# Performance work log

Hardware: AMD Instinct MI355X
Metric: run time of the kernel (lower is better)

The kernel has to match this reference:

```python
import jax, jax.numpy as jnp
import numpy as np

NUM_USERS = 100000
NUM_ITEMS = 50000
N_NODES = NUM_USERS + NUM_ITEMS
DIM = 64
N_LAYERS = 3
NNZ = 1000000
BATCH = 4096


def setup_inputs() -> dict:
    key = jax.random.key(0)
    k = jax.random.split(key, 7)
    user_idx = jax.random.randint(k[0], (BATCH,), 0, NUM_USERS, dtype=jnp.int64 if jax.config.jax_enable_x64 else jnp.int32)
    item_idx = jax.random.randint(k[1], (BATCH,), 0, NUM_ITEMS, dtype=jnp.int64 if jax.config.jax_enable_x64 else jnp.int32)
    rows = jax.random.randint(k[2], (NNZ,), 0, N_NODES, dtype=jnp.int32)
    cols = jax.random.randint(k[3], (NNZ,), 0, N_NODES, dtype=jnp.int32)
    values = jax.random.uniform(k[4], (NNZ,), dtype=jnp.float32)
    # embeddings initialized N(0, 1/dim) as in the torch module
    user_emb = jax.random.normal(k[5], (NUM_USERS, DIM), dtype=jnp.float32) / DIM
    item_emb = jax.random.normal(k[6], (NUM_ITEMS, DIM), dtype=jnp.float32) / DIM
    return {"user_idx": user_idx, "item_idx": item_idx, "rows": rows,
            "cols": cols, "values": values, "user_emb": user_emb, "item_emb": item_emb}


def _spmm(rows, cols, values, x):
    # sparse [N,N] @ dense [N,d] via gather + segment_sum
    gathered = values[:, None] * x[cols]            # [nnz, d]
    return jax.ops.segment_sum(gathered, rows, num_segments=N_NODES)


def _propagate(rows, cols, values, user_emb, item_emb):
    all_emb = jnp.concatenate([user_emb, item_emb], axis=0)  # [N, d]
    acc = all_emb
    for _ in range(N_LAYERS):
        all_emb = _spmm(rows, cols, values, all_emb)
        acc = acc + all_emb
    light_out = acc / jnp.asarray(N_LAYERS + 1, dtype=acc.dtype)  # mean over layers
    return light_out[:NUM_USERS], light_out[NUM_USERS:]


def reference(user_idx, item_idx, rows, cols, values, user_emb, item_emb):
    all_users, all_items = _propagate(rows, cols, values, user_emb, item_emb)
    user = all_users[user_idx]                      # [B, d]
    item = all_items[item_idx]                      # [B, d]
    rating = jnp.sum(user * item, axis=1)           # [B]
    return (rating, user, item)
```

## Files before the change

kernel.cpp:

```cpp
#include <hip/hip_runtime.h>

#define NUM_USERS 100000
#define NUM_ITEMS 50000
#define N_NODES   150000
#define DIM       64
#define NNZ       1000000
#define BATCH     4096

#define BROWS  240
#define NBUCK  (N_NODES / BROWS)
#define WPB    (BROWS / 8)
#define NWG    256
#define CHUNK  ((NNZ + NWG - 1) / NWG)
#define SCAN_N (NBUCK * NWG)
#define SCAN_B 512
#define NBLK_S ((SCAN_N + SCAN_B - 1) / SCAN_B)

#define NWAVES (NBUCK * WPB)
#define NBINS  32
#define ESCAP  4096
#define PACKED_CAP 3000000
#define CVB    2048

typedef unsigned int uint32;

__device__ __forceinline__ ushort f2bf(float f) {
    uint32 u = __float_as_uint(f);
    u += 0x7FFFu + ((u >> 16) & 1u);
    return (ushort)(u >> 16);
}
__device__ __forceinline__ float bf2f(ushort u) {
    return __uint_as_float(((uint32)u) << 16);
}

__global__ __launch_bounds__(256) void count_convert_kernel(
        const int* __restrict__ rows,
        int* __restrict__ cntArr,
        const float* __restrict__ user_emb,
        const float* __restrict__ item_emb,
        ushort* __restrict__ xb) {
    __shared__ int h[NBUCK];
    if (blockIdx.x < NWG) {
        for (int k = threadIdx.x; k < NBUCK; k += 256) h[k] = 0;
        __syncthreads();
        int lo = blockIdx.x * CHUNK, hi = min(NNZ, lo + CHUNK);
        for (int e = lo + threadIdx.x; e < hi; e += 256)
            atomicAdd(&h[__builtin_nontemporal_load(&rows[e]) / BROWS], 1);
        __syncthreads();
        for (int k = threadIdx.x; k < NBUCK; k += 256)
            cntArr[k * NWG + blockIdx.x] = h[k];
    } else {
        const int64_t total4 = (int64_t)N_NODES * DIM / 4;
        const int64_t user4  = (int64_t)NUM_USERS * DIM / 4;
        int64_t stride = (int64_t)CVB * 256;
        for (int64_t i = (int64_t)(blockIdx.x - NWG) * 256 + threadIdx.x;
             i < total4; i += stride) {
            float4 v = (i < user4) ? ((const float4*)user_emb)[i]
                                   : ((const float4*)item_emb)[i - user4];
            ushort4 o;
            o.x = f2bf(v.x); o.y = f2bf(v.y); o.z = f2bf(v.z); o.w = f2bf(v.w);
            ((ushort4*)xb)[i] = o;
        }
    }
}

__global__ __launch_bounds__(SCAN_B) void scan_block_kernel(
        const int* __restrict__ in, int* __restrict__ out,
        int* __restrict__ blksum, int n) {
    __shared__ int sh[SCAN_B];
    int i = blockIdx.x * SCAN_B + threadIdx.x;
    int v = (i < n) ? in[i] : 0;
    sh[threadIdx.x] = v;
    __syncthreads();
    for (int off = 1; off < SCAN_B; off <<= 1) {
        int t = (threadIdx.x >= off) ? sh[threadIdx.x - off] : 0;
        __syncthreads();
        sh[threadIdx.x] += t;
        __syncthreads();
    }
    if (i < n) out[i] = sh[threadIdx.x] - v;
    if (threadIdx.x == SCAN_B - 1) blksum[blockIdx.x] = sh[SCAN_B - 1];
}

__global__ __launch_bounds__(SCAN_B) void scan_top_kernel(int* __restrict__ blksum,
                                                          int nblk,
                                                          int* __restrict__ rowptr,
                                                          int* __restrict__ gcur) {
    __shared__ int sh[SCAN_B];
    int v = (threadIdx.x < nblk) ? blksum[threadIdx.x] : 0;
    sh[threadIdx.x] = v;
    __syncthreads();
    for (int off = 1; off < SCAN_B; off <<= 1) {
        int t = (threadIdx.x >= off) ? sh[threadIdx.x - off] : 0;
        __syncthreads();
        sh[threadIdx.x] += t;
        __syncthreads();
    }
    if (threadIdx.x < nblk) blksum[threadIdx.x] = sh[threadIdx.x] - v;
    if (threadIdx.x == 0) { rowptr[N_NODES] = NNZ; gcur[0] = 0; }
}

__global__ __launch_bounds__(256) void scatter_lds_kernel(
        const int* __restrict__ rows,
        const int* __restrict__ cols,
        const float* __restrict__ vals,
        const int* __restrict__ baseArr,
        const int* __restrict__ blksum,
        int2* __restrict__ ebuf) {
    __shared__ int cur[NBUCK];
    for (int k = threadIdx.x; k < NBUCK; k += 256) {
        int idx = k * NWG + blockIdx.x;
        cur[k] = baseArr[idx] + blksum[idx >> 9];
    }
    __syncthreads();
    int lo = blockIdx.x * CHUNK, hi = min(NNZ, lo + CHUNK);
    for (int e = lo + threadIdx.x; e < hi; e += 256) {
        int   r = __builtin_nontemporal_load(&rows[e]);
        int   c = __builtin_nontemporal_load(&cols[e]);
        float v = __builtin_nontemporal_load(&vals[e]);
        int   b = r / BROWS;
        int pos = atomicAdd(&cur[b], 1);
        ebuf[pos] = make_int2(((r - b * BROWS) << 18) | c, __float_as_int(v));
    }
}

__global__ __launch_bounds__(256) void buildpack_kernel(
        const int* __restrict__ baseArr,
        const int* __restrict__ blksum,
        const int2* __restrict__ ebuf,
        int2* __restrict__ ebuf2,
        int* __restrict__ rowptr,
        int* __restrict__ perm,
        int* __restrict__ tw,
        int* __restrict__ twb,
        int2* __restrict__ packed,
        int* __restrict__ gcur) {
    __shared__ int  cnt[BROWS];
    __shared__ int  rowofs[BROWS];
    __shared__ int  cur[BROWS];
    __shared__ int  sh[256];
    __shared__ int2 es[ESCAP];
    __shared__ int  sr[BROWS];
    __shared__ int  binc[NBINS];
    __shared__ int  binb[NBINS];
    __shared__ int  twq[WPB];
    __shared__ int  lofs[WPB];
    __shared__ int  baseSh;

    const int b   = blockIdx.x;
    const int tid = threadIdx.x;
    const int i0  = b * NWG;
    const int start = baseArr[i0] + blksum[i0 >> 9];
    const int i1  = (b + 1) * NWG;
    const int end = (b == NBUCK - 1) ? NNZ : (baseArr[i1] + blksum[i1 >> 9]);
    const int m   = end - start;

    for (int k = tid; k < BROWS; k += 256) cnt[k] = 0;
    if (tid < NBINS) binc[tid] = 0;
    __syncthreads();

    for (int e = start + tid; e < end; e += 256)
        atomicAdd(&cnt[ebuf[e].x >> 18], 1);
    __syncthreads();

    int v = (tid < BROWS) ? cnt[tid] : 0;
    sh[tid] = v;
    __syncthreads();
    for (int off = 1; off < 256; off <<= 1) {
        int t = (tid >= off) ? sh[tid - off] : 0;
        __syncthreads();
        sh[tid] += t;
        __syncthreads();
    }
    if (tid < BROWS) {
        int p = sh[tid] - v;
        rowofs[tid] = p;
        cur[tid] = p;
        rowptr[b * BROWS + tid] = start + p;
    }
    __syncthreads();

    for (int e = start + tid; e < end; e += 256) {
        int2 p = ebuf[e];
        int row8 = p.x >> 18;
        int col  = p.x & 0x3FFFF;
        int pos = atomicAdd(&cur[row8], 1);
        if (pos < ESCAP) es[pos] = make_int2(col, p.y);
    }
    __syncthreads();
    for (int k = tid; k < m; k += 256) ebuf2[start + k] = es[k];

    if (tid < BROWS) atomicAdd(&binc[min(cnt[tid], NBINS - 1)], 1);
    __syncthreads();
    if (tid == 0) {
        int s = 0;
        for (int k = 0; k < NBINS; ++k) { binb[k] = s; s += binc[k]; binc[k] = 0; }
    }
    __syncthreads();
    if (tid < BROWS) {
        int bin = min(cnt[tid], NBINS - 1);
        int idx = atomicAdd(&binc[bin], 1);
        sr[binb[bin] + idx] = tid;
    }
    __syncthreads();

    if (tid < WPB) {
        int T = 0;
        #pragma unroll
        for (int j = 0; j < 8; ++j) T = max(T, cnt[sr[8 * tid + j]]);
        twq[tid] = T;
    }
    __syncthreads();
    if (tid == 0) {
        int s = 0;
        for (int q = 0; q < WPB; ++q) { lofs[q] = s; s += twq[q]; }
        baseSh = atomicAdd(gcur, s);
    }
    __syncthreads();
    const int base = baseSh;

    if (tid < WPB) {
        tw[b * WPB + tid]  = twq[tid];
        twb[b * WPB + tid] = base + lofs[tid];
    }
    if (tid < BROWS) perm[b * BROWS + tid] = b * BROWS + sr[tid];

    for (int q = 0; q < WPB; ++q) {
        int T = twq[q];
        int64_t bq = (int64_t)(base + lofs[q]) * 8;
        for (int idx = tid; idx < 8 * T; idx += 256) {
            int t = idx >> 3, j = idx & 7;
            int row8 = sr[8 * q + j];
            int d = cnt[row8];
            int2 ed = (t < d) ? es[rowofs[row8] + t] : make_int2(0, 0);
            packed[bq + idx] = ed;
        }
    }
}

__global__ __launch_bounds__(256) void spmm8p_kernel(
        const int* __restrict__ perm,
        const int* __restrict__ twb,
        const int* __restrict__ tw,
        const long long* __restrict__ packed,
        const ushort* __restrict__ xin,
        ushort* __restrict__ yout) {
    int w = (int)((blockIdx.x * blockDim.x + threadIdx.x) >> 6);
    if (w >= NWAVES) return;
    const int lane = threadIdx.x & 63;
    const int j    = lane >> 3;
    const int sub8 = lane & 7;
    const int T = tw[w];
    const int64_t base = (int64_t)twb[w] * 8;
    const int rowv = perm[8 * w + j];
    const uint4* __restrict__ x4 = (const uint4*)xin;

    float acc[8] = {0.f, 0.f, 0.f, 0.f, 0.f, 0.f, 0.f, 0.f};

    #define DO_TRIP(tt)                                                        \
    {                                                                          \
        int   colsel = __shfl(edc, (tt) * 8 + j, 64);                          \
        float valsel = __uint_as_float((uint32)__shfl(edv, (tt) * 8 + j, 64)); \
        uint4 u = x4[(uint32)colsel * 8 + sub8];                               \
        acc[0] = fmaf(valsel, __uint_as_float(u.x << 16), acc[0]);             \
        acc[1] = fmaf(valsel, __uint_as_float(u.x & 0xFFFF0000u), acc[1]);     \
        acc[2] = fmaf(valsel, __uint_as_float(u.y << 16), acc[2]);             \
        acc[3] = fmaf(valsel, __uint_as_float(u.y & 0xFFFF0000u), acc[3]);     \
        acc[4] = fmaf(valsel, __uint_as_float(u.z << 16), acc[4]);             \
        acc[5] = fmaf(valsel, __uint_as_float(u.z & 0xFFFF0000u), acc[5]);     \
        acc[6] = fmaf(valsel, __uint_as_float(u.w << 16), acc[6]);             \
        acc[7] = fmaf(valsel, __uint_as_float(u.w & 0xFFFF0000u), acc[7]);     \
    }

    int t0 = 0;
    for (; t0 + 8 <= T; t0 += 8) {
        long long raw = __builtin_nontemporal_load(&packed[base + (int64_t)t0 * 8 + lane]);
        int edc = (int)(uint32)(raw & 0xFFFFFFFFll);
        int edv = (int)(uint32)(raw >> 32);
        DO_TRIP(0) DO_TRIP(1) DO_TRIP(2) DO_TRIP(3)
        DO_TRIP(4) DO_TRIP(5) DO_TRIP(6) DO_TRIP(7)
    }
    if (t0 < T) {
        long long raw = __builtin_nontemporal_load(&packed[base + (int64_t)t0 * 8 + lane]);
        int edc = (int)(uint32)(raw & 0xFFFFFFFFll);
        int edv = (int)(uint32)(raw >> 32);
        int rem = T - t0;
        for (int tt = 0; tt < rem; ++tt) DO_TRIP(tt)
    }
    #undef DO_TRIP

    uint4 o;
    o.x = (uint32)f2bf(acc[0]) | ((uint32)f2bf(acc[1]) << 16);
    o.y = (uint32)f2bf(acc[2]) | ((uint32)f2bf(acc[3]) << 16);
    o.z = (uint32)f2bf(acc[4]) | ((uint32)f2bf(acc[5]) << 16);
    o.w = (uint32)f2bf(acc[6]) | ((uint32)f2bf(acc[7]) << 16);
    ((uint4*)yout)[(uint32)rowv * 8 + sub8] = o;
}

__global__ __launch_bounds__(256) void batch_out_kernel(
        const int* __restrict__ user_idx,
        const int* __restrict__ item_idx,
        const int* __restrict__ rowptr,
        const int2* __restrict__ edges,
        const ushort* __restrict__ xin,
        const float* __restrict__ user_emb,
        const float* __restrict__ item_emb,
        const ushort* __restrict__ l1,
        const ushort* __restrict__ l2,
        float* __restrict__ out) {
    const int lane = threadIdx.x & 63;
    const int w = (int)(((uint32)blockIdx.x * blockDim.x + threadIdx.x) >> 6);
    const int i0 = w * 4;
    if (i0 >= BATCH) return;

    int rowv[8];
    int e[8], end[8];
    int trips = 0;
    #pragma unroll
    for (int j = 0; j < 8; ++j) {
        int row = (j < 4) ? user_idx[i0 + j]
                          : (NUM_USERS + item_idx[i0 + j - 4]);
        rowv[j] = row;
        e[j]   = rowptr[row];
        end[j] = rowptr[row + 1];
        trips = max(trips, end[j] - e[j]);
    }
    float a[8] = {0.f, 0.f, 0.f, 0.f, 0.f, 0.f, 0.f, 0.f};

    for (int t = 0; t < trips; ++t) {
        int   col[8];
        float val[8];
        #pragma unroll
        for (int j = 0; j < 8; ++j) {
            bool act = e[j] < end[j];
            int idx  = __builtin_amdgcn_readfirstlane(act ? e[j] : 0);
            int2 ed  = edges[idx];
            col[j] = __builtin_amdgcn_readfirstlane(ed.x);
            val[j] = act ? __int_as_float(ed.y) : 0.f;
            e[j]  += act ? 1 : 0;
        }
        #pragma unroll
        for (int j = 0; j < 8; ++j) {
            float xv = bf2f(xin[(int64_t)col[j] * DIM + lane]);
            a[j] = fmaf(val[j], xv, a[j]);
        }
    }

    float uvv[8];
    #pragma unroll
    for (int j = 0; j < 8; ++j) {
        int row = rowv[j];
        int64_t ro = (int64_t)row * DIM + lane;
        float emb = (j < 4) ? user_emb[ro]
                            : item_emb[(int64_t)(row - NUM_USERS) * DIM + lane];
        uvv[j] = (emb + bf2f(l1[ro]) + bf2f(l2[ro]) + a[j]) * 0.25f;
    }
    #pragma unroll
    for (int j = 0; j < 4; ++j)
        out[(int64_t)BATCH + (int64_t)(i0 + j) * DIM + lane] = uvv[j];
    #pragma unroll
    for (int j = 4; j < 8; ++j)
        out[(int64_t)BATCH + (int64_t)BATCH * DIM
            + (int64_t)(i0 + j - 4) * DIM + lane] = uvv[j];

    #pragma unroll
    for (int k = 0; k < 4; ++k) {
        float p = uvv[k] * uvv[k + 4];
        #pragma unroll
        for (int off = 32; off >= 1; off >>= 1) p += __shfl_down(p, off, 64);
        if (lane == 0) out[i0 + k] = p;
    }
}

extern "C" void kernel_launch(void* const* d_in, const int* in_sizes, int n_in,
                              void* d_out, int out_size, void* d_ws, size_t ws_size,
                              hipStream_t stream) {
    const int*   user_idx = (const int*)  d_in[0];
    const int*   item_idx = (const int*)  d_in[1];
    const int*   rows     = (const int*)  d_in[2];
    const int*   cols     = (const int*)  d_in[3];
    const float* vals     = (const float*)d_in[4];
    const float* user_emb = (const float*)d_in[5];
    const float* item_emb = (const float*)d_in[6];
    float*       out      = (float*)d_out;

    char* base = (char*)d_ws;
    size_t off = 0;
    auto alloc = [&](size_t bytes) -> char* {
        char* p = base + off;
        off = (off + bytes + 255) & ~(size_t)255;
        return p;
    };
    int*    cntArr  = (int*)   alloc((size_t)SCAN_N * sizeof(int));
    int*    baseArr = (int*)   alloc((size_t)SCAN_N * sizeof(int));
    int*    blksum  = (int*)   alloc((size_t)(NBLK_S + 1) * sizeof(int));
    int*    rowptr  = (int*)   alloc((size_t)(N_NODES + 1) * sizeof(int));
    int*    gcur    = (int*)   alloc((size_t)64 * sizeof(int));
    int2*   ebuf    = (int2*)  alloc((size_t)NNZ * sizeof(int2));
    int2*   ebuf2   = (int2*)  alloc((size_t)NNZ * sizeof(int2));
    int2*   packed  = (int2*)  alloc((size_t)PACKED_CAP * sizeof(int2));
    int*    perm    = (int*)   alloc((size_t)N_NODES * sizeof(int));
    int*    tw      = (int*)   alloc((size_t)NWAVES * sizeof(int));
    int*    twb     = (int*)   alloc((size_t)NWAVES * sizeof(int));
    ushort* xb      = (ushort*)alloc((size_t)N_NODES * DIM * sizeof(ushort));
    ushort* buf0    = (ushort*)alloc((size_t)N_NODES * DIM * sizeof(ushort));
    ushort* buf1    = (ushort*)alloc((size_t)N_NODES * DIM * sizeof(ushort));

    const int TB = 256;

    count_convert_kernel<<<NWG + CVB, TB, 0, stream>>>(
        rows, cntArr, user_emb, item_emb, xb);

    scan_block_kernel<<<NBLK_S, SCAN_B, 0, stream>>>(cntArr, baseArr, blksum, SCAN_N);
    scan_top_kernel<<<1, SCAN_B, 0, stream>>>(blksum, NBLK_S, rowptr, gcur);

    scatter_lds_kernel<<<NWG, TB, 0, stream>>>(rows, cols, vals, baseArr, blksum, ebuf);
    buildpack_kernel<<<NBUCK, TB, 0, stream>>>(
        baseArr, blksum, ebuf, ebuf2, rowptr, perm, tw, twb, packed, gcur);

    const int spmmBlocks = (NWAVES * 64 + TB - 1) / TB;
    spmm8p_kernel<<<spmmBlocks, TB, 0, stream>>>(
        perm, twb, tw, (const long long*)packed, xb, buf0);
    spmm8p_kernel<<<spmmBlocks, TB, 0, stream>>>(
        perm, twb, tw, (const long long*)packed, buf0, buf1);

    const int boBlocks = (BATCH / 4 * 64 + TB - 1) / TB;
    batch_out_kernel<<<boBlocks, TB, 0, stream>>>(
        user_idx, item_idx, rowptr, ebuf2, buf1,
        user_emb, item_emb, buf0, buf1, out);
}
```

Baseline: 128.9 us.

## Restrict second SpMM layer to rows reachable from batch nodes

```diff
diff --git a/kernel.cpp b/kernel.cpp
--- a/kernel.cpp
+++ b/kernel.cpp
@@ -15,12 +15,15 @@
 #define SCAN_N (NBUCK * NWG)
 #define SCAN_B 512
 #define NBLK_S ((SCAN_N + SCAN_B - 1) / SCAN_B)
+#define MARKB  ((2 * BATCH + SCAN_B - 1) / SCAN_B)
 
 #define NWAVES (NBUCK * WPB)
 #define NBINS  32
 #define ESCAP  4096
-#define PACKED_CAP 3000000
+#define PACKED_CAP  2500000
+#define PACKED2_CAP 1500000
 #define CVB    2048
+#define BMW    4704
 
 typedef unsigned int uint32;
 
@@ -38,7 +41,9 @@
         int* __restrict__ cntArr,
         const float* __restrict__ user_emb,
         const float* __restrict__ item_emb,
-        ushort* __restrict__ xb) {
+        ushort* __restrict__ xb,
+        uint32* __restrict__ bbm,
+        uint32* __restrict__ fbm) {
     __shared__ int h[NBUCK];
     if (blockIdx.x < NWG) {
         for (int k = threadIdx.x; k < NBUCK; k += 256) h[k] = 0;
@@ -49,7 +54,7 @@
         __syncthreads();
         for (int k = threadIdx.x; k < NBUCK; k += 256)
             cntArr[k * NWG + blockIdx.x] = h[k];
-    } else {
+    } else if (blockIdx.x < NWG + CVB) {
         const int64_t total4 = (int64_t)N_NODES * DIM / 4;
         const int64_t user4  = (int64_t)NUM_USERS * DIM / 4;
         int64_t stride = (int64_t)CVB * 256;
@@ -61,12 +66,24 @@
             o.x = f2bf(v.x); o.y = f2bf(v.y); o.z = f2bf(v.z); o.w = f2bf(v.w);
             ((ushort4*)xb)[i] = o;
         }
+    } else {
+        for (int k = threadIdx.x; k < BMW; k += 256) { bbm[k] = 0; fbm[k] = 0; }
     }
 }
 
 __global__ __launch_bounds__(SCAN_B) void scan_block_kernel(
         const int* __restrict__ in, int* __restrict__ out,
-        int* __restrict__ blksum, int n) {
+        int* __restrict__ blksum, int n,
+        const int* __restrict__ user_idx, const int* __restrict__ item_idx,
+        uint32* __restrict__ bbm) {
+    if (blockIdx.x >= NBLK_S) {
+        int i = (int)(blockIdx.x - NBLK_S) * SCAN_B + threadIdx.x;
+        if (i < 2 * BATCH) {
+            int row = (i < BATCH) ? user_idx[i] : (NUM_USERS + item_idx[i - BATCH]);
+            atomicOr(&bbm[row >> 5], 1u << (row & 31));
+        }
+        return;
+    }
     __shared__ int sh[SCAN_B];
     int i = blockIdx.x * SCAN_B + threadIdx.x;
     int v = (i < n) ? in[i] : 0;
@@ -97,7 +114,10 @@
         __syncthreads();
     }
     if (threadIdx.x < nblk) blksum[threadIdx.x] = sh[threadIdx.x] - v;
-    if (threadIdx.x == 0) { rowptr[N_NODES] = NNZ; gcur[0] = 0; }
+    if (threadIdx.x == 0) {
+        rowptr[N_NODES] = NNZ;
+        gcur[0] = 0; gcur[1] = 0; gcur[2] = 0; gcur[3] = NWAVES;
+    }
 }
 
 __global__ __launch_bounds__(256) void scatter_lds_kernel(
@@ -106,6 +126,8 @@
         const float* __restrict__ vals,
         const int* __restrict__ baseArr,
         const int* __restrict__ blksum,
+        const uint32* __restrict__ bbm,
+        uint32* __restrict__ fbm,
         int2* __restrict__ ebuf) {
     __shared__ int cur[NBUCK];
     for (int k = threadIdx.x; k < NBUCK; k += 256) {
@@ -118,6 +140,8 @@
         int   r = __builtin_nontemporal_load(&rows[e]);
         int   c = __builtin_nontemporal_load(&cols[e]);
         float v = __builtin_nontemporal_load(&vals[e]);
+        if ((bbm[r >> 5] >> (r & 31)) & 1u)
+            atomicOr(&fbm[c >> 5], 1u << (c & 31));
         int   b = r / BROWS;
         int pos = atomicAdd(&cur[b], 1);
         ebuf[pos] = make_int2(((r - b * BROWS) << 18) | c, __float_as_int(v));
@@ -134,6 +158,12 @@
         int* __restrict__ tw,
         int* __restrict__ twb,
         int2* __restrict__ packed,
+        const uint32* __restrict__ bbm,
+        const uint32* __restrict__ fbm,
+        int* __restrict__ perm2,
+        int* __restrict__ tw2,
+        int* __restrict__ twb2,
+        int2* __restrict__ packed2,
         int* __restrict__ gcur) {
     __shared__ int  cnt[BROWS];
     __shared__ int  rowofs[BROWS];
@@ -141,11 +171,12 @@
     __shared__ int  sh[256];
     __shared__ int2 es[ESCAP];
     __shared__ int  sr[BROWS];
+    __shared__ int  sr2[BROWS];
     __shared__ int  binc[NBINS];
     __shared__ int  binb[NBINS];
     __shared__ int  twq[WPB];
     __shared__ int  lofs[WPB];
-    __shared__ int  baseSh;
+    __shared__ int  baseSh, nfSh, baseW2, baseS2;
 
     const int b   = blockIdx.x;
     const int tid = threadIdx.x;
@@ -214,7 +245,7 @@
     if (tid == 0) {
         int s = 0;
         for (int q = 0; q < WPB; ++q) { lofs[q] = s; s += twq[q]; }
-        baseSh = atomicAdd(gcur, s);
+        baseSh = atomicAdd(&gcur[0], s);
     }
     __syncthreads();
     const int base = baseSh;
@@ -236,6 +267,69 @@
             packed[bq + idx] = ed;
         }
     }
+    __syncthreads();
+
+    if (tid < BROWS) {
+        int row = b * BROWS + tid;
+        cur[tid] = (int)(((bbm[row >> 5] | fbm[row >> 5]) >> (row & 31)) & 1u);
+    }
+    __syncthreads();
+    int v2 = (tid < BROWS) ? cur[sr[tid]] : 0;
+    sh[tid] = v2;
+    __syncthreads();
+    for (int off = 1; off < 256; off <<= 1) {
+        int t = (tid >= off) ? sh[tid - off] : 0;
+        __syncthreads();
+        sh[tid] += t;
+        __syncthreads();
+    }
+    if (tid < BROWS && v2) sr2[sh[tid] - 1] = sr[tid];
+    if (tid == 255) nfSh = sh[255];
+    __syncthreads();
+    const int nf = nfSh;
+    const int nwav2 = (nf + 7) >> 3;
+
+    if (tid < nwav2) {
+        int T = 0;
+        #pragma unroll
+        for (int j = 0; j < 8; ++j) {
+            int s = 8 * tid + j;
+            if (s < nf) T = max(T, cnt[sr2[s]]);
+        }
+        twq[tid] = T;
+    }
+    __syncthreads();
+    if (tid == 0) {
+        int s = 0;
+        for (int q = 0; q < nwav2; ++q) { lofs[q] = s; s += twq[q]; }
+        baseW2 = nwav2 ? atomicAdd(&gcur[2], nwav2) : 0;
+        baseS2 = s     ? atomicAdd(&gcur[1], s)     : 0;
+    }
+    __syncthreads();
+    if (tid < nwav2) {
+        tw2[baseW2 + tid]  = twq[tid];
+        twb2[baseW2 + tid] = baseS2 + lofs[tid];
+    }
+    if (tid < 8 * nwav2) {
+        int s = tid;
+        perm2[(int64_t)(baseW2 + (s >> 3)) * 8 + (s & 7)] =
+            (s < nf) ? b * BROWS + sr2[s] : N_NODES;
+    }
+    for (int q = 0; q < nwav2; ++q) {
+        int T = twq[q];
+        int64_t bq = (int64_t)(baseS2 + lofs[q]) * 8;
+        for (int idx = tid; idx < 8 * T; idx += 256) {
+            int t = idx >> 3, j = idx & 7;
+            int s = 8 * q + j;
+            int2 ed = make_int2(0, 0);
+            if (s < nf) {
+                int row8 = sr2[s];
+                int d = cnt[row8];
+                if (t < d) ed = es[rowofs[row8] + t];
+            }
+            packed2[bq + idx] = ed;
+        }
+    }
 }
 
 __global__ __launch_bounds__(256) void spmm8p_kernel(
@@ -244,9 +338,10 @@
         const int* __restrict__ tw,
         const long long* __restrict__ packed,
         const ushort* __restrict__ xin,
-        ushort* __restrict__ yout) {
+        ushort* __restrict__ yout,
+        const int* __restrict__ nwave) {
     int w = (int)((blockIdx.x * blockDim.x + threadIdx.x) >> 6);
-    if (w >= NWAVES) return;
+    if (w >= nwave[0]) return;
     const int lane = threadIdx.x & 63;
     const int j    = lane >> 3;
     const int sub8 = lane & 7;
@@ -396,33 +491,42 @@
     int*    blksum  = (int*)   alloc((size_t)(NBLK_S + 1) * sizeof(int));
     int*    rowptr  = (int*)   alloc((size_t)(N_NODES + 1) * sizeof(int));
     int*    gcur    = (int*)   alloc((size_t)64 * sizeof(int));
+    uint32* bbm     = (uint32*)alloc((size_t)BMW * sizeof(uint32));
+    uint32* fbm     = (uint32*)alloc((size_t)BMW * sizeof(uint32));
     int2*   ebuf    = (int2*)  alloc((size_t)NNZ * sizeof(int2));
     int2*   ebuf2   = (int2*)  alloc((size_t)NNZ * sizeof(int2));
     int2*   packed  = (int2*)  alloc((size_t)PACKED_CAP * sizeof(int2));
+    int2*   packed2 = (int2*)  alloc((size_t)PACKED2_CAP * sizeof(int2));
     int*    perm    = (int*)   alloc((size_t)N_NODES * sizeof(int));
+    int*    perm2   = (int*)   alloc((size_t)N_NODES * sizeof(int));
     int*    tw      = (int*)   alloc((size_t)NWAVES * sizeof(int));
     int*    twb     = (int*)   alloc((size_t)NWAVES * sizeof(int));
+    int*    tw2     = (int*)   alloc((size_t)NWAVES * sizeof(int));
+    int*    twb2    = (int*)   alloc((size_t)NWAVES * sizeof(int));
     ushort* xb      = (ushort*)alloc((size_t)N_NODES * DIM * sizeof(ushort));
     ushort* buf0    = (ushort*)alloc((size_t)N_NODES * DIM * sizeof(ushort));
-    ushort* buf1    = (ushort*)alloc((size_t)N_NODES * DIM * sizeof(ushort));
+    ushort* buf1    = (ushort*)alloc((size_t)(N_NODES + 8) * DIM * sizeof(ushort));
 
     const int TB = 256;
 
-    count_convert_kernel<<<NWG + CVB, TB, 0, stream>>>(
-        rows, cntArr, user_emb, item_emb, xb);
-
-    scan_block_kernel<<<NBLK_S, SCAN_B, 0, stream>>>(cntArr, baseArr, blksum, SCAN_N);
+    count_convert_kernel<<<NWG + CVB + 1, TB, 0, stream>>>(
+        rows, cntArr, user_emb, item_emb, xb, bbm, fbm);
+
+    scan_block_kernel<<<NBLK_S + MARKB, SCAN_B, 0, stream>>>(
+        cntArr, baseArr, blksum, SCAN_N, user_idx, item_idx, bbm);
     scan_top_kernel<<<1, SCAN_B, 0, stream>>>(blksum, NBLK_S, rowptr, gcur);
 
-    scatter_lds_kernel<<<NWG, TB, 0, stream>>>(rows, cols, vals, baseArr, blksum, ebuf);
+    scatter_lds_kernel<<<NWG, TB, 0, stream>>>(
+        rows, cols, vals, baseArr, blksum, bbm, fbm, ebuf);
     buildpack_kernel<<<NBUCK, TB, 0, stream>>>(
-        baseArr, blksum, ebuf, ebuf2, rowptr, perm, tw, twb, packed, gcur);
+        baseArr, blksum, ebuf, ebuf2, rowptr, perm, tw, twb, packed,
+        bbm, fbm, perm2, tw2, twb2, packed2, gcur);
 
     const int spmmBlocks = (NWAVES * 64 + TB - 1) / TB;
     spmm8p_kernel<<<spmmBlocks, TB, 0, stream>>>(
-        perm, twb, tw, (const long long*)packed, xb, buf0);
+        perm, twb, tw, (const long long*)packed, xb, buf0, gcur + 3);
     spmm8p_kernel<<<spmmBlocks, TB, 0, stream>>>(
-        perm, twb, tw, (const long long*)packed, buf0, buf1);
+        perm2, twb2, tw2, (const long long*)packed2, buf0, buf1, gcur + 2);
 
     const int boBlocks = (BATCH / 4 * 64 + TB - 1) / TB;
     batch_out_kernel<<<boBlocks, TB, 0, stream>>>(
```

Measured after the change: 140.6 us. 1.09x slower.
